# Performance work log

Measured on AMD Instinct MI355X. Metric: run time of the kernel, lower is better.

The kernel has to match this reference:

```python
import jax, jax.numpy as jnp
import numpy as np

NUM_HEADS = 16
THETA = 10000.0


def _rope(x, pos):
    # x: (B, H, S, d_k), pos: (B, S) int
    d_k = x.shape[-1]
    freqs = 1.0 / (THETA ** (jnp.arange(0, d_k, 2, dtype=jnp.float32) / d_k))  # (d_k/2,)
    angles = pos[..., None].astype(jnp.float32) * freqs  # (B, S, d_k/2)
    cos = jnp.cos(angles)[:, None, :, :]  # (B, 1, S, d_k/2) broadcast over heads
    sin = jnp.sin(angles)[:, None, :, :]
    x1 = x[..., 0::2]
    x2 = x[..., 1::2]
    out1 = x1 * cos - x2 * sin
    out2 = x1 * sin + x2 * cos
    # interleave back: (..., d_k/2, 2) -> (..., d_k)
    return jnp.stack((out1, out2), axis=-1).reshape(x.shape)


def setup_inputs() -> dict:
    key = jax.random.key(0)
    ks = jax.random.split(key, 6)
    B, S, D = 4, 2048, 1024
    x = jax.random.normal(ks[0], (B, S, D), dtype=jnp.float32)
    token_positions = jnp.sort(jax.random.randint(ks[1], (B, S), 0, S), axis=-1).astype(jnp.int32)
    Wq = jax.random.normal(ks[2], (D, D), dtype=jnp.float32) * (D ** -0.5)
    Wk = jax.random.normal(ks[3], (D, D), dtype=jnp.float32) * (D ** -0.5)
    Wv = jax.random.normal(ks[4], (D, D), dtype=jnp.float32) * (D ** -0.5)
    Wo = jax.random.normal(ks[5], (D, D), dtype=jnp.float32) * (D ** -0.5)
    return {"x": x, "token_positions": token_positions, "Wq": Wq, "Wk": Wk, "Wv": Wv, "Wo": Wo}


def reference(x, token_positions, Wq, Wk, Wv, Wo):
    B, S, D = x.shape
    H = NUM_HEADS
    d_k = D // H
    # projections: y = x @ W.T  (Linear stores weight as (d_out, d_in))
    q = jnp.einsum('bsd,od->bso', x, Wq).reshape(B, S, H, d_k).transpose(0, 2, 1, 3)
    k = jnp.einsum('bsd,od->bso', x, Wk).reshape(B, S, H, d_k).transpose(0, 2, 1, 3)
    v = jnp.einsum('bsd,od->bso', x, Wv).reshape(B, S, H, d_k).transpose(0, 2, 1, 3)
    q = _rope(q, token_positions)
    k = _rope(k, token_positions)
    scores = jnp.einsum('bhqd,bhkd->bhqk', q, k) / jnp.sqrt(jnp.float32(d_k))
    causal = jnp.tril(jnp.ones((S, S), dtype=bool))
    scores = jnp.where(causal, scores, -jnp.inf)
    attn = jax.nn.softmax(scores, axis=-1)
    attn = jnp.nan_to_num(attn, nan=0.0)
    out = jnp.einsum('bhqk,bhkd->bhqd', attn, v)
    out = out.transpose(0, 2, 1, 3).reshape(B, S, D)
    return jnp.einsum('bso,do->bsd', out, Wo)
```

## Files before the change

kernel.cpp:

```cpp
#include <hip/hip_runtime.h>
#include <stdint.h>

#define SEQ 2048
#define NH  16
#define DK  64
#define DM  1024
#define C2SM 0.18033688011112042f

typedef __bf16 bf16x8 __attribute__((ext_vector_type(8)));
typedef float  f32x4  __attribute__((ext_vector_type(4)));
typedef float  f32x16 __attribute__((ext_vector_type(16)));
typedef int    iv2    __attribute__((ext_vector_type(2)));
typedef void __attribute__((address_space(3))) lds_void;
typedef const void __attribute__((address_space(1))) glb_void;

__device__ __forceinline__ unsigned short f2b(float f) {
  unsigned int u = __float_as_uint(f);
  u += 0x7fffu + ((u >> 16) & 1u);
  return (unsigned short)(u >> 16);
}
__device__ __forceinline__ float b2f(unsigned short h) {
  return __uint_as_float(((unsigned int)h) << 16);
}
__device__ __forceinline__ void gload_lds16(const void* g, void* lds) {
  __builtin_amdgcn_global_load_lds((glb_void*)(uintptr_t)g,
                                   (lds_void*)(unsigned int)(uintptr_t)lds,
                                   16, 0, 0);
}
__device__ __forceinline__ unsigned int cvtpk(float lo, float hi) {
  unsigned int r;
  asm("v_cvt_pk_bf16_f32 %0, %1, %2" : "=v"(r) : "v"(lo), "v"(hi));
  return r;
}
__device__ __forceinline__ iv2 pl32swap(int a, int b) {
  return __builtin_amdgcn_permlane32_swap(a, b, false, false);
}

__global__ __launch_bounds__(256) void k_cvt(const float* __restrict__ src,
                                             unsigned short* __restrict__ dst, int n4) {
  int i = blockIdx.x * 256 + threadIdx.x;
  if (i >= n4) return;
  float4 v = ((const float4*)src)[i];
  uint2 o;
  o.x = (unsigned int)f2b(v.x) | ((unsigned int)f2b(v.y) << 16);
  o.y = (unsigned int)f2b(v.z) | ((unsigned int)f2b(v.w) << 16);
  ((uint2*)dst)[i] = o;
}

__global__ __launch_bounds__(256) void k_cvtw(const float* __restrict__ w0,
                                              const float* __restrict__ w1,
                                              const float* __restrict__ w2,
                                              const float* __restrict__ w3,
                                              unsigned short* __restrict__ dst) {
  int i = blockIdx.x * 256 + threadIdx.x;
  const float* s = (i < 524288) ? ((i < 262144) ? w0 : w1)
                                : ((i < 786432) ? w2 : w3);
  float4 v = ((const float4*)s)[i & 262143];
  uint2 o;
  o.x = (unsigned int)f2b(v.x) | ((unsigned int)f2b(v.y) << 16);
  o.y = (unsigned int)f2b(v.z) | ((unsigned int)f2b(v.w) << 16);
  ((uint2*)dst)[i] = o;
}

__global__ __launch_bounds__(256) void k_tab(float2* __restrict__ tab) {
  int i = blockIdx.x * 256 + threadIdx.x;
  int p = i >> 5, f = i & 31;
  float freq = powf(10000.0f, -(float)(2 * f) / (float)DK);
  float ang = (float)p * freq;
  tab[i] = make_float2(cosf(ang), sinf(ang));
}

template <int MODE>
__global__ __launch_bounds__(256) void k_gemm(const unsigned short* __restrict__ A,
                                              const unsigned short* __restrict__ B,
                                              void* __restrict__ C, void* __restrict__ C2,
                                              const int* __restrict__ pos,
                                              const float2* __restrict__ tab,
                                              int M, int N, int K) {
  __shared__ __align__(16) unsigned short As[3][4096];
  __shared__ __align__(16) unsigned short Bs[3][4096];
  const int tid = threadIdx.x;
  const int wid = tid >> 6, lane = tid & 63;
  const int lr = lane & 15, lk = lane >> 4;
  const int wr = wid >> 1, wc = wid & 1;
  const int m0 = blockIdx.x * 128, n0 = blockIdx.y * 128;
  const int r0 = tid >> 2;
  const int csw = (((tid & 3) ^ ((r0 >> 1) & 3)) << 3);
  const int ss = ((lk ^ ((lr >> 1) & 3)) << 3);
  f32x4 acc[4][4] = {};

#define GSTAGE(bi, k0)                                                       \
  do {                                                                       \
    gload_lds16(A + (size_t)(m0 + r0) * K + (k0) + csw, &As[bi][wid * 512]); \
    gload_lds16(A + (size_t)(m0 + 64 + r0) * K + (k0) + csw,                 \
                &As[bi][2048 + wid * 512]);                                  \
    gload_lds16(B + (size_t)(n0 + r0) * K + (k0) + csw, &Bs[bi][wid * 512]); \
    gload_lds16(B + (size_t)(n0 + 64 + r0) * K + (k0) + csw,                 \
                &Bs[bi][2048 + wid * 512]);                                  \
  } while (0)

  const int nt = K >> 5;
  GSTAGE(0, 0);
  if (nt > 1) {
    GSTAGE(1, 32);
    asm volatile("s_waitcnt vmcnt(4)" ::: "memory");
  } else {
    asm volatile("s_waitcnt vmcnt(0)" ::: "memory");
  }
  __builtin_amdgcn_s_barrier();
  int c0 = 0, c1 = 1, c2 = 2;
  for (int t = 0; t < nt; ++t) {
    if (t + 2 < nt) GSTAGE(c2, (t + 2) * 32);
    bf16x8 af[4], bfv[4];
#pragma unroll
    for (int i = 0; i < 4; ++i)
      af[i] = *(const bf16x8*)&As[c0][(wr * 64 + i * 16 + lr) * 32 + ss];
#pragma unroll
    for (int j = 0; j < 4; ++j)
      bfv[j] = *(const bf16x8*)&Bs[c0][(wc * 64 + j * 16 + lr) * 32 + ss];
    __builtin_amdgcn_s_setprio(1);
#pragma unroll
    for (int i = 0; i < 4; ++i)
#pragma unroll
      for (int j = 0; j < 4; ++j)
        acc[i][j] = __builtin_amdgcn_mfma_f32_16x16x32_bf16(af[i], bfv[j], acc[i][j], 0, 0, 0);
    __builtin_amdgcn_s_setprio(0);
    if (t + 1 < nt) {
      if (t + 2 < nt)
        asm volatile("s_waitcnt vmcnt(4)" ::: "memory");
      else
        asm volatile("s_waitcnt vmcnt(0)" ::: "memory");
      __builtin_amdgcn_s_barrier();
    }
    int tmp = c0; c0 = c1; c1 = c2; c2 = tmp;
  }
#undef GSTAGE

  if (MODE == 1) {
#pragma unroll
    for (int i = 0; i < 4; ++i) {
      const int rbase = m0 + wr * 64 + i * 16 + lk * 4;
#pragma unroll
      for (int j = 0; j < 4; ++j) {
        const int col = n0 + wc * 64 + j * 16 + lr;
#pragma unroll
        for (int r = 0; r < 4; ++r)
          ((float*)C)[(size_t)(rbase + r) * N + col] = acc[i][j][r];
      }
    }
  } else {
    const int tt = n0 >> 10;
    if (tt == 2) {
#pragma unroll
      for (int i = 0; i < 4; ++i) {
        const int rbase = m0 + wr * 64 + i * 16 + lk * 4;
        const int bb = rbase >> 11;
#pragma unroll
        for (int j = 0; j < 4; ++j) {
          const int col = n0 + wc * 64 + j * 16 + lr;
          const int h = (col >> 6) & 15, d = col & 63;
#pragma unroll
          for (int r = 0; r < 4; ++r) {
            const int s = (rbase + r) & (SEQ - 1);
            ((unsigned short*)C2)[((((size_t)bb * NH + h) * SEQ) + s) * DK + d] =
                f2b(acc[i][j][r]);
          }
        }
      }
    } else {
#pragma unroll
      for (int i = 0; i < 4; ++i) {
        const int rbase = m0 + wr * 64 + i * 16 + lk * 4;
        const int bb = rbase >> 11;
        int prr[4];
#pragma unroll
        for (int r = 0; r < 4; ++r)
          prr[r] = pos[bb * SEQ + ((rbase + r) & (SEQ - 1))];
#pragma unroll
        for (int j = 0; j < 4; ++j) {
          const int col = n0 + wc * 64 + j * 16 + lr;
          const int h = (col >> 6) & 15, d = col & 63;
          const int f = d >> 1;
#pragma unroll
          for (int r = 0; r < 4; ++r) {
            float v = acc[i][j][r];
            float pv = __shfl_xor(v, 1);
            float2 cs = tab[(size_t)prr[r] * 32 + f];
            float o = (d & 1) ? __builtin_fmaf(pv, cs.y, v * cs.x)
                              : __builtin_fmaf(-pv, cs.y, v * cs.x);
            const int s = (rbase + r) & (SEQ - 1);
            ((unsigned short*)C)[(size_t)tt * 8388608 +
                                 ((((size_t)bb * NH + h) * SEQ) + s) * DK + d] = f2b(o);
          }
        }
      }
    }
  }
}

__global__ __launch_bounds__(256) void k_vt(const unsigned short* __restrict__ V,
                                            unsigned short* __restrict__ VT) {
  __shared__ __align__(16) unsigned short T[64 * 64];
  const int bh = blockIdx.y, st = blockIdx.x;
  const unsigned short* Vp = V + (size_t)bh * SEQ * DK + (size_t)st * 64 * DK;
  unsigned short* Tp = VT + (size_t)bh * DK * SEQ + st * 64;
#pragma unroll
  for (int it = 0; it < 2; ++it) {
    int c = it * 256 + threadIdx.x;
    int s = c >> 3, slot = c & 7;
    uint4 v = *(const uint4*)&Vp[s * DK + slot * 8];
    *(uint4*)&T[s * 64 + ((slot ^ (s & 7)) << 3)] = v;
  }
  __syncthreads();
#pragma unroll
  for (int it = 0; it < 2; ++it) {
    int c = it * 256 + threadIdx.x;
    int d = c >> 3, sq = (c & 7) << 3;
    unsigned int w[4];
#pragma unroll
    for (int k = 0; k < 4; ++k) {
      int r0 = sq + 2 * k, r1 = sq + 2 * k + 1;
      unsigned int lo = T[r0 * 64 + ((((d >> 3) ^ (r0 & 7)) << 3) | (d & 7))];
      unsigned int hi = T[r1 * 64 + ((((d >> 3) ^ (r1 & 7)) << 3) | (d & 7))];
      w[k] = lo | (hi << 16);
    }
    *(uint4*)&Tp[(size_t)d * SEQ + sq] = make_uint4(w[0], w[1], w[2], w[3]);
  }
}

__global__ __launch_bounds__(256) void k_attn(const unsigned short* __restrict__ Q,
                                              const unsigned short* __restrict__ K,
                                              const unsigned short* __restrict__ VT,
                                              unsigned short* __restrict__ O) {
  __shared__ __align__(16) unsigned short Ks[2][64 * 64];
  __shared__ __align__(16) unsigned short Vs[2][64 * 64];
  const int tid = threadIdx.x, wid = tid >> 6, lane = tid & 63;
  const int l31 = lane & 31, hi = lane >> 5;
  const int bh = blockIdx.y;
  const unsigned short* Qp = Q + (size_t)bh * SEQ * DK;
  const unsigned short* Kp = K + (size_t)bh * SEQ * DK;
  const unsigned short* Vp = VT + (size_t)bh * DK * SEQ;
  const int b = bh >> 4, h = bh & (NH - 1);
  const int srow0 = tid >> 3, srow1 = 32 + (tid >> 3);
  const int sslot0 = (tid & 7) ^ (srow0 & 7), sslot1 = (tid & 7) ^ (srow1 & 7);

#define STAGE(bi, kb)                                                               \
  do {                                                                              \
    gload_lds16(Kp + (size_t)((kb) + srow0) * DK + sslot0 * 8, &Ks[bi][wid * 512]); \
    gload_lds16(Kp + (size_t)((kb) + srow1) * DK + sslot1 * 8,                      \
                &Ks[bi][2048 + wid * 512]);                                         \
    gload_lds16(Vp + (size_t)srow0 * SEQ + (kb) + sslot0 * 8, &Vs[bi][wid * 512]);  \
    gload_lds16(Vp + (size_t)srow1 * SEQ + (kb) + sslot1 * 8,                       \
                &Vs[bi][2048 + wid * 512]);                                         \
  } while (0)

#pragma unroll
  for (int pass = 0; pass < 2; ++pass) {
    const int qt = pass ? 15 - (int)blockIdx.x : (int)blockIdx.x;
    const int q0 = qt * 128;
    const int qw = q0 + wid * 32;
    const int qrow = qw + l31;
    bf16x8 qf[4];
#pragma unroll
    for (int ks = 0; ks < 4; ++ks)
      qf[ks] = *(const bf16x8*)&Qp[(size_t)qrow * DK + ks * 16 + hi * 8];
    f32x16 oacc[2] = {};
    float m_ = -1e30f, l_ = 0.f;
    const int ntiles = 2 * qt + 2;
    STAGE(0, 0);
    for (int kt = 0; kt < ntiles; ++kt) {
      const int cur = kt & 1;
      const int kb = kt * 64;
      if (kt + 1 < ntiles) {
        STAGE(cur ^ 1, kb + 64);
        asm volatile("s_waitcnt vmcnt(4)" ::: "memory");
      } else {
        asm volatile("s_waitcnt vmcnt(0)" ::: "memory");
      }
      __builtin_amdgcn_s_barrier();
      if (kb <= qw + 31) {
        f32x16 sa[2];
        __builtin_amdgcn_s_setprio(1);
#pragma unroll
        for (int kg = 0; kg < 2; ++kg) {
          const int krow = kg * 32 + l31;
          f32x16 z = {};
#pragma unroll
          for (int ks = 0; ks < 4; ++ks) {
            bf16x8 kf = *(const bf16x8*)((const char*)&Ks[cur][0] + krow * 128 +
                                         (((2 * ks + hi) ^ (krow & 7)) << 4));
            z = __builtin_amdgcn_mfma_f32_32x32x16_bf16(kf, qf[ks], z, 0, 0, 0);
          }
          sa[kg] = z;
        }
        __builtin_amdgcn_s_setprio(0);
        if (kb + 64 > qw) {
          const int th0 = qrow - kb - 4 * hi;
#pragma unroll
          for (int kg = 0; kg < 2; ++kg) {
            const int th = th0 - kg * 32;
#pragma unroll
            for (int r = 0; r < 16; ++r) {
              const int cst = (r & 3) + 8 * (r >> 2);
              if (cst > th) sa[kg][r] = -1e30f;
            }
          }
        }
        float mx;
        {
          float a0 = fmaxf(fmaxf(sa[0][0], sa[0][1]), fmaxf(sa[0][2], sa[0][3]));
          float a1 = fmaxf(fmaxf(sa[0][4], sa[0][5]), fmaxf(sa[0][6], sa[0][7]));
          float a2 = fmaxf(fmaxf(sa[0][8], sa[0][9]), fmaxf(sa[0][10], sa[0][11]));
          float a3 = fmaxf(fmaxf(sa[0][12], sa[0][13]), fmaxf(sa[0][14], sa[0][15]));
          float a4 = fmaxf(fmaxf(sa[1][0], sa[1][1]), fmaxf(sa[1][2], sa[1][3]));
          float a5 = fmaxf(fmaxf(sa[1][4], sa[1][5]), fmaxf(sa[1][6], sa[1][7]));
          float a6 = fmaxf(fmaxf(sa[1][8], sa[1][9]), fmaxf(sa[1][10], sa[1][11]));
          float a7 = fmaxf(fmaxf(sa[1][12], sa[1][13]), fmaxf(sa[1][14], sa[1][15]));
          mx = fmaxf(fmaxf(fmaxf(a0, a1), fmaxf(a2, a3)),
                     fmaxf(fmaxf(a4, a5), fmaxf(a6, a7)));
          iv2 t = pl32swap(__float_as_int(mx), __float_as_int(mx));
          mx = fmaxf(__int_as_float(t.x), __int_as_float(t.y));
        }
        if (!__all(mx <= m_ + 16.f)) {
          const float mn = fmaxf(m_, mx);
          const float sc = __builtin_amdgcn_exp2f((m_ - mn) * C2SM);
          m_ = mn;
          l_ *= sc;
#pragma unroll
          for (int vg = 0; vg < 2; ++vg)
#pragma unroll
            for (int r = 0; r < 16; ++r) oacc[vg][r] *= sc;
        }
        const float mc = m_ * C2SM;
        float sum = 0.f;
#pragma unroll
        for (int kg = 0; kg < 2; ++kg)
#pragma unroll
          for (int r = 0; r < 16; ++r) {
            const float p = __builtin_amdgcn_exp2f(__builtin_fmaf(sa[kg][r], C2SM, -mc));
            sa[kg][r] = p;
            sum += p;
          }
        {
          iv2 t = pl32swap(__float_as_int(sum), __float_as_int(sum));
          l_ += __int_as_float(t.x) + __int_as_float(t.y);
        }
        __builtin_amdgcn_s_setprio(1);
#pragma unroll
        for (int kg = 0; kg < 2; ++kg)
#pragma unroll
          for (int ks2 = 0; ks2 < 2; ++ks2) {
            const int rb = ks2 * 8;
            unsigned wA = cvtpk(sa[kg][rb + 0], sa[kg][rb + 1]);
            unsigned wB = cvtpk(sa[kg][rb + 4], sa[kg][rb + 5]);
            unsigned wC = cvtpk(sa[kg][rb + 2], sa[kg][rb + 3]);
            unsigned wD = cvtpk(sa[kg][rb + 6], sa[kg][rb + 7]);
            iv2 r0 = pl32swap((int)wA, (int)wB);
            iv2 r1 = pl32swap((int)wC, (int)wD);
            union { uint4 u; bf16x8 v; } pu;
            pu.u = make_uint4((unsigned)r0.x, (unsigned)r1.x, (unsigned)r0.y, (unsigned)r1.y);
            const int ks = kg * 2 + ks2;
#pragma unroll
            for (int vg = 0; vg < 2; ++vg) {
              const int vrow = vg * 32 + l31;
              bf16x8 vf = *(const bf16x8*)((const char*)&Vs[cur][0] + vrow * 128 +
                                           (((2 * ks + hi) ^ (vrow & 7)) << 4));
              oacc[vg] = __builtin_amdgcn_mfma_f32_32x32x16_bf16(vf, pu.v, oacc[vg], 0, 0, 0);
            }
          }
        __builtin_amdgcn_s_setprio(0);
      }
      __builtin_amdgcn_s_barrier();
    }
    const float inv = 1.0f / l_;
    unsigned short* Orow = O + ((size_t)(b * SEQ + qrow)) * DM + h * DK;
#pragma unroll
    for (int vg = 0; vg < 2; ++vg)
#pragma unroll
      for (int j = 0; j < 4; ++j) {
        unsigned lo = cvtpk(oacc[vg][4 * j + 0] * inv, oacc[vg][4 * j + 1] * inv);
        unsigned hh = cvtpk(oacc[vg][4 * j + 2] * inv, oacc[vg][4 * j + 3] * inv);
        *(uint2*)&Orow[vg * 32 + 8 * j + 4 * hi] = make_uint2(lo, hh);
      }
  }
#undef STAGE
}

extern "C" void kernel_launch(void* const* d_in, const int* in_sizes, int n_in,
                              void* d_out, int out_size, void* d_ws, size_t ws_size,
                              hipStream_t stream) {
  const float* x = (const float*)d_in[0];
  const int* tp = (const int*)d_in[1];
  const float* W[4] = {(const float*)d_in[2], (const float*)d_in[3],
                       (const float*)d_in[4], (const float*)d_in[5]};
  unsigned short* xb = (unsigned short*)d_ws;
  unsigned short* wb0 = xb + (size_t)8192 * 1024;
  unsigned short* wb3 = wb0 + (size_t)3 * 1024 * 1024;
  float2* tab = (float2*)(wb0 + (size_t)4 * 1024 * 1024);
  unsigned short* Qb = (unsigned short*)(tab + SEQ * 32);
  unsigned short* Kb = Qb + (size_t)8192 * 1024;
  unsigned short* VTb = Kb + (size_t)8192 * 1024;
  unsigned short* Ob = VTb + (size_t)8192 * 1024;
  unsigned short* Vb = Ob;

  k_cvt<<<8192, 256, 0, stream>>>(x, xb, 2097152);
  k_cvtw<<<4096, 256, 0, stream>>>(W[0], W[1], W[2], W[3], wb0);
  k_tab<<<256, 256, 0, stream>>>(tab);
  k_gemm<3><<<dim3(64, 24), 256, 0, stream>>>(xb, wb0, Qb, Vb, tp, tab, 8192, 3072, 1024);
  k_vt<<<dim3(32, 64), 256, 0, stream>>>(Vb, VTb);
  k_attn<<<dim3(8, 4 * NH), 256, 0, stream>>>(Qb, Kb, VTb, Ob);
  k_gemm<1><<<dim3(64, 8), 256, 0, stream>>>(Ob, wb3, d_out, nullptr, nullptr, nullptr,
                                             8192, 1024, 1024);
}
```

Before: 181.6 us.

## Double attention KV tile to 128 keys and flatten grid indexing

Each attention iteration now stages and processes 128 keys instead of 64, which halves the loop trips, barriers and online-softmax rescale checks per query tile. The V tile swizzle is widened to 16 slots to match the 256-byte rows. The grid becomes 1D with the head index in the low bits, so blocks that share K/V are launched close together, which may improve L2 reuse. In exchange, LDS use doubles to 64KB, register pressure rises from holding four score accumulators, and the diagonal tiles waste more masked work.

```diff
diff --git a/kernel.cpp b/kernel.cpp
--- a/kernel.cpp
+++ b/kernel.cpp
@@ -34,6 +34,13 @@
 }
 __device__ __forceinline__ iv2 pl32swap(int a, int b) {
   return __builtin_amdgcn_permlane32_swap(a, b, false, false);
+}
+__device__ __forceinline__ float vmax16(const f32x16& v) {
+  float a0 = fmaxf(fmaxf(v[0], v[1]), fmaxf(v[2], v[3]));
+  float a1 = fmaxf(fmaxf(v[4], v[5]), fmaxf(v[6], v[7]));
+  float a2 = fmaxf(fmaxf(v[8], v[9]), fmaxf(v[10], v[11]));
+  float a3 = fmaxf(fmaxf(v[12], v[13]), fmaxf(v[14], v[15]));
+  return fmaxf(fmaxf(a0, a1), fmaxf(a2, a3));
 }
 
 __global__ __launch_bounds__(256) void k_cvt(const float* __restrict__ src,
@@ -232,33 +239,34 @@
                                               const unsigned short* __restrict__ K,
                                               const unsigned short* __restrict__ VT,
                                               unsigned short* __restrict__ O) {
-  __shared__ __align__(16) unsigned short Ks[2][64 * 64];
-  __shared__ __align__(16) unsigned short Vs[2][64 * 64];
+  __shared__ __align__(16) unsigned short Ks[2][128 * 64];
+  __shared__ __align__(16) unsigned short Vs[2][64 * 128];
   const int tid = threadIdx.x, wid = tid >> 6, lane = tid & 63;
   const int l31 = lane & 31, hi = lane >> 5;
-  const int bh = blockIdx.y;
+  const int n = blockIdx.x;
+  const int x = n >> 6, bh = n & 63;
   const unsigned short* Qp = Q + (size_t)bh * SEQ * DK;
   const unsigned short* Kp = K + (size_t)bh * SEQ * DK;
   const unsigned short* Vp = VT + (size_t)bh * DK * SEQ;
   const int b = bh >> 4, h = bh & (NH - 1);
-  const int srow0 = tid >> 3, srow1 = 32 + (tid >> 3);
-  const int sslot0 = (tid & 7) ^ (srow0 & 7), sslot1 = (tid & 7) ^ (srow1 & 7);
-
-#define STAGE(bi, kb)                                                               \
-  do {                                                                              \
-    gload_lds16(Kp + (size_t)((kb) + srow0) * DK + sslot0 * 8, &Ks[bi][wid * 512]); \
-    gload_lds16(Kp + (size_t)((kb) + srow1) * DK + sslot1 * 8,                      \
-                &Ks[bi][2048 + wid * 512]);                                         \
-    gload_lds16(Vp + (size_t)srow0 * SEQ + (kb) + sslot0 * 8, &Vs[bi][wid * 512]);  \
-    gload_lds16(Vp + (size_t)srow1 * SEQ + (kb) + sslot1 * 8,                       \
-                &Vs[bi][2048 + wid * 512]);                                         \
+
+#define STAGE(bi, kb)                                                           \
+  do {                                                                          \
+    _Pragma("unroll") for (int rp = 0; rp < 4; ++rp) {                          \
+      const int c = rp * 256 + tid;                                             \
+      const int kr = c >> 3, ko = ((c & 7) ^ (kr & 7)) << 3;                    \
+      const int vr = c >> 4, vo = ((c & 15) ^ (vr & 15)) << 3;                  \
+      gload_lds16(Kp + (size_t)((kb) + kr) * DK + ko,                           \
+                  &Ks[bi][rp * 2048 + wid * 512]);                              \
+      gload_lds16(Vp + (size_t)vr * SEQ + (kb) + vo,                            \
+                  &Vs[bi][rp * 2048 + wid * 512]);                              \
+    }                                                                           \
   } while (0)
 
 #pragma unroll
   for (int pass = 0; pass < 2; ++pass) {
-    const int qt = pass ? 15 - (int)blockIdx.x : (int)blockIdx.x;
-    const int q0 = qt * 128;
-    const int qw = q0 + wid * 32;
+    const int qt = pass ? 15 - x : x;
+    const int qw = qt * 128 + wid * 32;
     const int qrow = qw + l31;
     bf16x8 qf[4];
 #pragma unroll
@@ -266,23 +274,23 @@
       qf[ks] = *(const bf16x8*)&Qp[(size_t)qrow * DK + ks * 16 + hi * 8];
     f32x16 oacc[2] = {};
     float m_ = -1e30f, l_ = 0.f;
-    const int ntiles = 2 * qt + 2;
+    const int ntiles = qt + 1;
     STAGE(0, 0);
     for (int kt = 0; kt < ntiles; ++kt) {
       const int cur = kt & 1;
-      const int kb = kt * 64;
+      const int kb = kt << 7;
       if (kt + 1 < ntiles) {
-        STAGE(cur ^ 1, kb + 64);
-        asm volatile("s_waitcnt vmcnt(4)" ::: "memory");
+        STAGE(cur ^ 1, kb + 128);
+        asm volatile("s_waitcnt vmcnt(8)" ::: "memory");
       } else {
         asm volatile("s_waitcnt vmcnt(0)" ::: "memory");
       }
       __builtin_amdgcn_s_barrier();
       if (kb <= qw + 31) {
-        f32x16 sa[2];
+        f32x16 sa[4];
         __builtin_amdgcn_s_setprio(1);
 #pragma unroll
-        for (int kg = 0; kg < 2; ++kg) {
+        for (int kg = 0; kg < 4; ++kg) {
           const int krow = kg * 32 + l31;
           f32x16 z = {};
 #pragma unroll
@@ -294,10 +302,10 @@
           sa[kg] = z;
         }
         __builtin_amdgcn_s_setprio(0);
-        if (kb + 64 > qw) {
+        if (kb + 128 > qw) {
           const int th0 = qrow - kb - 4 * hi;
 #pragma unroll
-          for (int kg = 0; kg < 2; ++kg) {
+          for (int kg = 0; kg < 4; ++kg) {
             const int th = th0 - kg * 32;
 #pragma unroll
             for (int r = 0; r < 16; ++r) {
@@ -306,18 +314,9 @@
             }
           }
         }
-        float mx;
+        float mx = fmaxf(fmaxf(vmax16(sa[0]), vmax16(sa[1])),
+                         fmaxf(vmax16(sa[2]), vmax16(sa[3])));
         {
-          float a0 = fmaxf(fmaxf(sa[0][0], sa[0][1]), fmaxf(sa[0][2], sa[0][3]));
-          float a1 = fmaxf(fmaxf(sa[0][4], sa[0][5]), fmaxf(sa[0][6], sa[0][7]));
-          float a2 = fmaxf(fmaxf(sa[0][8], sa[0][9]), fmaxf(sa[0][10], sa[0][11]));
-          float a3 = fmaxf(fmaxf(sa[0][12], sa[0][13]), fmaxf(sa[0][14], sa[0][15]));
-          float a4 = fmaxf(fmaxf(sa[1][0], sa[1][1]), fmaxf(sa[1][2], sa[1][3]));
-          float a5 = fmaxf(fmaxf(sa[1][4], sa[1][5]), fmaxf(sa[1][6], sa[1][7]));
-          float a6 = fmaxf(fmaxf(sa[1][8], sa[1][9]), fmaxf(sa[1][10], sa[1][11]));
-          float a7 = fmaxf(fmaxf(sa[1][12], sa[1][13]), fmaxf(sa[1][14], sa[1][15]));
-          mx = fmaxf(fmaxf(fmaxf(a0, a1), fmaxf(a2, a3)),
-                     fmaxf(fmaxf(a4, a5), fmaxf(a6, a7)));
           iv2 t = pl32swap(__float_as_int(mx), __float_as_int(mx));
           mx = fmaxf(__int_as_float(t.x), __int_as_float(t.y));
         }
@@ -334,7 +333,7 @@
         const float mc = m_ * C2SM;
         float sum = 0.f;
 #pragma unroll
-        for (int kg = 0; kg < 2; ++kg)
+        for (int kg = 0; kg < 4; ++kg)
 #pragma unroll
           for (int r = 0; r < 16; ++r) {
             const float p = __builtin_amdgcn_exp2f(__builtin_fmaf(sa[kg][r], C2SM, -mc));
@@ -347,7 +346,7 @@
         }
         __builtin_amdgcn_s_setprio(1);
 #pragma unroll
-        for (int kg = 0; kg < 2; ++kg)
+        for (int kg = 0; kg < 4; ++kg)
 #pragma unroll
           for (int ks2 = 0; ks2 < 2; ++ks2) {
             const int rb = ks2 * 8;
@@ -363,8 +362,8 @@
 #pragma unroll
             for (int vg = 0; vg < 2; ++vg) {
               const int vrow = vg * 32 + l31;
-              bf16x8 vf = *(const bf16x8*)((const char*)&Vs[cur][0] + vrow * 128 +
-                                           (((2 * ks + hi) ^ (vrow & 7)) << 4));
+              bf16x8 vf = *(const bf16x8*)((const char*)&Vs[cur][0] + vrow * 256 +
+                                           (((2 * ks + hi) ^ (vrow & 15)) << 4));
               oacc[vg] = __builtin_amdgcn_mfma_f32_32x32x16_bf16(vf, pu.v, oacc[vg], 0, 0, 0);
             }
           }
@@ -408,7 +407,7 @@
   k_tab<<<256, 256, 0, stream>>>(tab);
   k_gemm<3><<<dim3(64, 24), 256, 0, stream>>>(xb, wb0, Qb, Vb, tp, tab, 8192, 3072, 1024);
   k_vt<<<dim3(32, 64), 256, 0, stream>>>(Vb, VTb);
-  k_attn<<<dim3(8, 4 * NH), 256, 0, stream>>>(Qb, Kb, VTb, Ob);
+  k_attn<<<512, 256, 0, stream>>>(Qb, Kb, VTb, Ob);
   k_gemm<1><<<dim3(64, 8), 256, 0, stream>>>(Ob, wb3, d_out, nullptr, nullptr, nullptr,
                                              8192, 1024, 1024);
 }
```

Measured after the change: 198.7 us. 9.4% more time.

## Shrink attention blocks to 64 query rows with 2 waves, 1024 blocks

Applied to the files above, without the earlier changes.

The attention kernel now uses 128-thread blocks (2 waves) covering 64 query rows per pass instead of 256 threads covering 128 rows. The grid becomes 1024 one-dimensional blocks with the (batch, head) index in the low bits, so neighbouring blocks share K/V. The causal skip test is removed because every wave now needs every K tile up to the diagonal. The aim is more blocks for load balance and occupancy and less wasted causal work per block, at the cost of loading each K/V tile once per 64 query rows instead of once per 128, which doubles global/LDS staging traffic.

```diff
diff --git a/kernel.cpp b/kernel.cpp
--- a/kernel.cpp
+++ b/kernel.cpp
@@ -228,7 +228,7 @@
   }
 }
 
-__global__ __launch_bounds__(256) void k_attn(const unsigned short* __restrict__ Q,
+__global__ __launch_bounds__(128) void k_attn(const unsigned short* __restrict__ Q,
                                               const unsigned short* __restrict__ K,
                                               const unsigned short* __restrict__ VT,
                                               unsigned short* __restrict__ O) {
@@ -236,29 +236,29 @@
   __shared__ __align__(16) unsigned short Vs[2][64 * 64];
   const int tid = threadIdx.x, wid = tid >> 6, lane = tid & 63;
   const int l31 = lane & 31, hi = lane >> 5;
-  const int bh = blockIdx.y;
+  const int n = blockIdx.x;
+  const int bh = n & 63, x = n >> 6;
   const unsigned short* Qp = Q + (size_t)bh * SEQ * DK;
   const unsigned short* Kp = K + (size_t)bh * SEQ * DK;
   const unsigned short* Vp = VT + (size_t)bh * DK * SEQ;
   const int b = bh >> 4, h = bh & (NH - 1);
-  const int srow0 = tid >> 3, srow1 = 32 + (tid >> 3);
-  const int sslot0 = (tid & 7) ^ (srow0 & 7), sslot1 = (tid & 7) ^ (srow1 & 7);
-
-#define STAGE(bi, kb)                                                               \
-  do {                                                                              \
-    gload_lds16(Kp + (size_t)((kb) + srow0) * DK + sslot0 * 8, &Ks[bi][wid * 512]); \
-    gload_lds16(Kp + (size_t)((kb) + srow1) * DK + sslot1 * 8,                      \
-                &Ks[bi][2048 + wid * 512]);                                         \
-    gload_lds16(Vp + (size_t)srow0 * SEQ + (kb) + sslot0 * 8, &Vs[bi][wid * 512]);  \
-    gload_lds16(Vp + (size_t)srow1 * SEQ + (kb) + sslot1 * 8,                       \
-                &Vs[bi][2048 + wid * 512]);                                         \
+
+#define STAGE(bi, kb)                                                          \
+  do {                                                                         \
+    _Pragma("unroll") for (int i = 0; i < 4; ++i) {                            \
+      const int c = i * 128 + tid;                                             \
+      const int row = c >> 3, sl = ((c & 7) ^ (row & 7)) << 3;                 \
+      gload_lds16(Kp + (size_t)((kb) + row) * DK + sl,                         \
+                  &Ks[bi][(i * 128 + wid * 64) * 8]);                          \
+      gload_lds16(Vp + (size_t)row * SEQ + (kb) + sl,                          \
+                  &Vs[bi][(i * 128 + wid * 64) * 8]);                          \
+    }                                                                          \
   } while (0)
 
 #pragma unroll
   for (int pass = 0; pass < 2; ++pass) {
-    const int qt = pass ? 15 - (int)blockIdx.x : (int)blockIdx.x;
-    const int q0 = qt * 128;
-    const int qw = q0 + wid * 32;
+    const int qt = pass ? 31 - x : x;
+    const int qw = qt * 64 + wid * 32;
     const int qrow = qw + l31;
     bf16x8 qf[4];
 #pragma unroll
@@ -266,19 +266,19 @@
       qf[ks] = *(const bf16x8*)&Qp[(size_t)qrow * DK + ks * 16 + hi * 8];
     f32x16 oacc[2] = {};
     float m_ = -1e30f, l_ = 0.f;
-    const int ntiles = 2 * qt + 2;
+    const int ntiles = qt + 1;
     STAGE(0, 0);
     for (int kt = 0; kt < ntiles; ++kt) {
       const int cur = kt & 1;
       const int kb = kt * 64;
       if (kt + 1 < ntiles) {
         STAGE(cur ^ 1, kb + 64);
-        asm volatile("s_waitcnt vmcnt(4)" ::: "memory");
+        asm volatile("s_waitcnt vmcnt(8)" ::: "memory");
       } else {
         asm volatile("s_waitcnt vmcnt(0)" ::: "memory");
       }
       __builtin_amdgcn_s_barrier();
-      if (kb <= qw + 31) {
+      {
         f32x16 sa[2];
         __builtin_amdgcn_s_setprio(1);
 #pragma unroll
@@ -408,7 +408,7 @@
   k_tab<<<256, 256, 0, stream>>>(tab);
   k_gemm<3><<<dim3(64, 24), 256, 0, stream>>>(xb, wb0, Qb, Vb, tp, tab, 8192, 3072, 1024);
   k_vt<<<dim3(32, 64), 256, 0, stream>>>(Vb, VTb);
-  k_attn<<<dim3(8, 4 * NH), 256, 0, stream>>>(Qb, Kb, VTb, Ob);
+  k_attn<<<1024, 128, 0, stream>>>(Qb, Kb, VTb, Ob);
   k_gemm<1><<<dim3(64, 8), 256, 0, stream>>>(Ob, wb3, d_out, nullptr, nullptr, nullptr,
                                              8192, 1024, 1024);
 }
```

Measured after the change: 181.0 us. No clear change (-0.3%).
